# Kernel tuning notes

Hardware: AMD Instinct MI355X
Metric: run time of the kernel (lower is better)

The kernel has to match this reference:

```python
import jax, jax.numpy as jnp
import numpy as np

D_MODEL = 768
N_HEADS = 12
CHUNK = 512
N_LM = 32
BATCH = 2
SEQ = 8192


def setup_inputs() -> dict:
    key = jax.random.key(0)
    ks = jax.random.split(key, 9)
    s = 1.0 / np.sqrt(D_MODEL)
    return {
        "x": jax.random.normal(ks[0], (BATCH, SEQ, D_MODEL), jnp.float32),
        "Wq": jax.random.normal(ks[1], (D_MODEL, D_MODEL), jnp.float32) * s,
        "bq": jax.random.normal(ks[2], (D_MODEL,), jnp.float32) * 0.01,
        "Wk": jax.random.normal(ks[3], (D_MODEL, D_MODEL), jnp.float32) * s,
        "bk": jax.random.normal(ks[4], (D_MODEL,), jnp.float32) * 0.01,
        "Wv": jax.random.normal(ks[5], (D_MODEL, D_MODEL), jnp.float32) * s,
        "bv": jax.random.normal(ks[6], (D_MODEL,), jnp.float32) * 0.01,
        "Wo": jax.random.normal(ks[7], (D_MODEL, D_MODEL), jnp.float32) * s,
        "bo": jax.random.normal(ks[8], (D_MODEL,), jnp.float32) * 0.01,
    }


def reference(x, Wq, bq, Wk, bk, Wv, bv, Wo, bo):
    B, S, D = x.shape
    H, hd = N_HEADS, D // N_HEADS
    scale = hd ** -0.5
    n_chunks = S // CHUNK  # SEQ chosen divisible by CHUNK -> no padding path

    # Global landmarks: mean-pool over N_LM evenly spaced segments
    seg = S // N_LM
    lm = x[:, : seg * N_LM, :].reshape(B, N_LM, seg, D).mean(axis=2)  # (B, L, D)

    # Q over local tokens only
    q = (x @ Wq.T + bq).reshape(B, n_chunks, CHUNK, H, hd)

    # K/V over [landmarks ++ local chunk]
    xc = x.reshape(B, n_chunks, CHUNK, D)
    lm_exp = jnp.broadcast_to(lm[:, None], (B, n_chunks, N_LM, D))
    kv = jnp.concatenate([lm_exp, xc], axis=2)  # (B, n_chunks, N_LM+CHUNK, D)
    k = (kv @ Wk.T + bk).reshape(B, n_chunks, N_LM + CHUNK, H, hd)
    v = (kv @ Wv.T + bv).reshape(B, n_chunks, N_LM + CHUNK, H, hd)

    attn = jnp.einsum("bnqhd,bnkhd->bnhqk", q, k) * scale
    attn = jax.nn.softmax(attn, axis=-1)  # dropout=0 (eval)
    out = jnp.einsum("bnhqk,bnkhd->bnqhd", attn, v).reshape(B, S, D)
    return out @ Wo.T + bo
```

## Files before the change

kernel.cpp:

```cpp
#include <hip/hip_runtime.h>
#include <cstdint>
#include <cstddef>

#define D_MODEL 768
#define N_HEADS 12
#define HEAD_DIM 64
#define CHUNK_SZ 512
#define N_LM 32
#define BATCH 2
#define SEQ 8192
#define N_CH 16
#define SEG 256
#define TOK (BATCH*SEQ)
#define MKV_PAD 16512
#define QSCALE 0.18033688011112042f
#define DEFER_THR 12.0f

typedef unsigned short u16;
typedef __attribute__((ext_vector_type(8))) __bf16 bf16x8;
typedef __attribute__((ext_vector_type(4))) float f32x4;

__device__ __forceinline__ u16 f2bf_rn(float f){
  union { __bf16 b; u16 u; } c; c.b = (__bf16)f; return c.u;
}

__global__ __launch_bounds__(256) void cvt4_kernel(
    const float* __restrict__ w0, const float* __restrict__ w1,
    const float* __restrict__ w2, const float* __restrict__ w3,
    u16* __restrict__ o0, u16* __restrict__ o1, u16* __restrict__ o2, u16* __restrict__ o3)
{
  const int n4 = D_MODEL*D_MODEL/4;
  int i = blockIdx.x*256 + threadIdx.x;
  int sel = i / n4, j = i - sel*n4;
  const float* s = sel==0 ? w0 : sel==1 ? w1 : sel==2 ? w2 : w3;
  u16* o = sel==0 ? o0 : sel==1 ? o1 : sel==2 ? o2 : o3;
  float4 v = reinterpret_cast<const float4*>(s)[j];
  ushort4 p; p.x=f2bf_rn(v.x); p.y=f2bf_rn(v.y); p.z=f2bf_rn(v.z); p.w=f2bf_rn(v.w);
  reinterpret_cast<ushort4*>(o)[j] = p;
}

__global__ void build_xcat_kernel(const float* __restrict__ x, u16* __restrict__ xcat){
  const int total4 = MKV_PAD * D_MODEL / 4;
  const int x4 = TOK * D_MODEL / 4;
  int stride = gridDim.x * blockDim.x;
  for (int i = blockIdx.x*blockDim.x + threadIdx.x; i < total4; i += stride){
    ushort4 o;
    if (i < x4){
      float4 v = reinterpret_cast<const float4*>(x)[i];
      o.x = f2bf_rn(v.x); o.y = f2bf_rn(v.y); o.z = f2bf_rn(v.z); o.w = f2bf_rn(v.w);
    } else { o.x = 0; o.y = 0; o.z = 0; o.w = 0; }
    reinterpret_cast<ushort4*>(xcat)[i] = o;
  }
}

__global__ __launch_bounds__(256) void lm_part_kernel(const float* __restrict__ x, float* __restrict__ lmp){
  int seg = blockIdx.x >> 3, sub = blockIdx.x & 7;
  int b = seg >> 5, l = seg & 31;
  const float* base = x + ((size_t)b*SEQ + (size_t)l*SEG + (size_t)sub*32) * D_MODEL;
  int d = threadIdx.x;
  float a0=0.f, a1=0.f, a2=0.f;
  for (int tt=0; tt<32; ++tt){
    const float* row = base + (size_t)tt*D_MODEL;
    a0 += row[d]; a1 += row[d+256]; a2 += row[d+512];
  }
  float* orow = lmp + (size_t)blockIdx.x * D_MODEL;
  orow[d] = a0; orow[d+256] = a1; orow[d+512] = a2;
}
__global__ __launch_bounds__(256) void lm_final_kernel(const float* __restrict__ lmp, u16* __restrict__ xcat){
  int seg = blockIdx.x;
  int d = threadIdx.x;
  float a0=0.f, a1=0.f, a2=0.f;
  #pragma unroll
  for (int i=0;i<8;i++){
    const float* p = lmp + ((size_t)seg*8 + i)*D_MODEL;
    a0 += p[d]; a1 += p[d+256]; a2 += p[d+512];
  }
  u16* orow = xcat + ((size_t)TOK + seg)*D_MODEL;
  const float inv = 1.f/(float)SEG;
  orow[d] = f2bf_rn(a0*inv); orow[d+256] = f2bf_rn(a1*inv); orow[d+512] = f2bf_rn(a2*inv);
}

template<int OUT_F32, int BIAS_ROW>
__global__ __launch_bounds__(256) void gemm_bt_kernel(
    const u16* __restrict__ A, const u16* __restrict__ Bt,
    const float* __restrict__ bias, void* __restrict__ Cout, int ldc, float scale)
{
  __shared__ u16 As[128][72];
  __shared__ u16 Bs[128][72];
  const int t = threadIdx.x;
  const int lane = t & 63, wid = t >> 6;
  const int wr = wid >> 1, wc = wid & 1;
  const int lr = lane & 15, lg = lane >> 4;
  const size_t row0 = (size_t)blockIdx.y * 128;
  const int col0 = blockIdx.x * 128;

  f32x4 acc[4][4];
  #pragma unroll
  for (int m=0;m<4;m++)
    #pragma unroll
    for (int n=0;n<4;n++) acc[m][n] = f32x4{0.f,0.f,0.f,0.f};

  const int sc = (t & 7) << 3;
  const int sr0 = t >> 3;

  for (int ko = 0; ko < D_MODEL; ko += 64){
    #pragma unroll
    for (int i=0;i<4;i++){
      int r = sr0 + i*32;
      *reinterpret_cast<float4*>(&As[r][sc]) =
        *reinterpret_cast<const float4*>(&A[(row0 + r)*D_MODEL + ko + sc]);
      *reinterpret_cast<float4*>(&Bs[r][sc]) =
        *reinterpret_cast<const float4*>(&Bt[((size_t)col0 + r)*D_MODEL + ko + sc]);
    }
    __syncthreads();
    #pragma unroll
    for (int kk=0;kk<2;kk++){
      bf16x8 af[4], bv[4];
      #pragma unroll
      for (int m=0;m<4;m++)
        af[m] = *reinterpret_cast<const bf16x8*>(&As[wr*64 + m*16 + lr][kk*32 + lg*8]);
      #pragma unroll
      for (int n=0;n<4;n++)
        bv[n] = *reinterpret_cast<const bf16x8*>(&Bs[wc*64 + n*16 + lr][kk*32 + lg*8]);
      #pragma unroll
      for (int m=0;m<4;m++)
        #pragma unroll
        for (int n=0;n<4;n++)
          acc[m][n] = __builtin_amdgcn_mfma_f32_16x16x32_bf16(af[m], bv[n], acc[m][n], 0, 0, 0);
    }
    __syncthreads();
  }

  #pragma unroll
  for (int m=0;m<4;m++){
    #pragma unroll
    for (int n=0;n<4;n++){
      const int col = col0 + wc*64 + n*16 + lr;
      const float bcol = BIAS_ROW ? 0.f : bias[col];
      #pragma unroll
      for (int e=0;e<4;e++){
        size_t row = row0 + wr*64 + m*16 + lg*4 + e;
        float b = BIAS_ROW ? bias[row] : bcol;
        float val = (acc[m][n][e] + b) * scale;
        if (OUT_F32) reinterpret_cast<float*>(Cout)[row*(size_t)ldc + col] = val;
        else         reinterpret_cast<u16*>(Cout)[row*(size_t)ldc + col] = f2bf_rn(val);
      }
    }
  }
}

__global__ __launch_bounds__(256) void gemm_qk_kernel(
    const u16* __restrict__ A, const u16* __restrict__ Wqk,
    const float* __restrict__ bq, const float* __restrict__ bk,
    u16* __restrict__ Qb, u16* __restrict__ Kb)
{
  __shared__ u16 As[128][72];
  __shared__ u16 Bs[128][72];
  const int t = threadIdx.x;
  const int lane = t & 63, wid = t >> 6;
  const int wr = wid >> 1, wc = wid & 1;
  const int lr = lane & 15, lg = lane >> 4;
  const size_t row0 = (size_t)blockIdx.y * 128;
  const int col0 = blockIdx.x * 128;
  const bool isk = col0 >= 768;

  f32x4 acc[4][4];
  #pragma unroll
  for (int m=0;m<4;m++)
    #pragma unroll
    for (int n=0;n<4;n++) acc[m][n] = f32x4{0.f,0.f,0.f,0.f};

  const int sc = (t & 7) << 3;
  const int sr0 = t >> 3;

  for (int ko = 0; ko < D_MODEL; ko += 64){
    #pragma unroll
    for (int i=0;i<4;i++){
      int r = sr0 + i*32;
      *reinterpret_cast<float4*>(&As[r][sc]) =
        *reinterpret_cast<const float4*>(&A[(row0 + r)*D_MODEL + ko + sc]);
      *reinterpret_cast<float4*>(&Bs[r][sc]) =
        *reinterpret_cast<const float4*>(&Wqk[((size_t)col0 + r)*D_MODEL + ko + sc]);
    }
    __syncthreads();
    #pragma unroll
    for (int kk=0;kk<2;kk++){
      bf16x8 af[4], bv[4];
      #pragma unroll
      for (int m=0;m<4;m++)
        af[m] = *reinterpret_cast<const bf16x8*>(&As[wr*64 + m*16 + lr][kk*32 + lg*8]);
      #pragma unroll
      for (int n=0;n<4;n++)
        bv[n] = *reinterpret_cast<const bf16x8*>(&Bs[wc*64 + n*16 + lr][kk*32 + lg*8]);
      #pragma unroll
      for (int m=0;m<4;m++)
        #pragma unroll
        for (int n=0;n<4;n++)
          acc[m][n] = __builtin_amdgcn_mfma_f32_16x16x32_bf16(af[m], bv[n], acc[m][n], 0, 0, 0);
    }
    __syncthreads();
  }

  const float scale = isk ? 1.f : QSCALE;
  u16* dst = isk ? Kb : Qb;
  #pragma unroll
  for (int m=0;m<4;m++){
    #pragma unroll
    for (int n=0;n<4;n++){
      const int col = col0 + wc*64 + n*16 + lr;
      const int ocol = isk ? col - 768 : col;
      const float b = isk ? bk[ocol] : bq[ocol];
      #pragma unroll
      for (int e=0;e<4;e++){
        size_t row = row0 + wr*64 + m*16 + lg*4 + e;
        if (isk || row < TOK){
          float val = (acc[m][n][e] + b) * scale;
          dst[row*D_MODEL + ocol] = f2bf_rn(val);
        }
      }
    }
  }
}

template<int NK>
__device__ __forceinline__ void attn_compute(
    int lr, int lg,
    const u16 (* __restrict__ Ks)[72], const u16 (* __restrict__ Vs)[72],
    u16 (* __restrict__ Pw)[72],
    const bf16x8 (&qf)[2][2], float (&m_run)[2], float (&l_run)[2], f32x4 (&of)[2][4])
{
  constexpr int NCF = NK/16;
  constexpr int NKT = NK/32;

  f32x4 s2[2][NCF];
  #pragma unroll
  for (int c=0;c<NCF;c++){
    bf16x8 kf0 = *reinterpret_cast<const bf16x8*>(&Ks[c*16 + lr][lg*8]);
    bf16x8 kf1 = *reinterpret_cast<const bf16x8*>(&Ks[c*16 + lr][32 + lg*8]);
    #pragma unroll
    for (int r=0;r<2;r++){
      f32x4 s = f32x4{0.f,0.f,0.f,0.f};
      s = __builtin_amdgcn_mfma_f32_16x16x32_bf16(kf0, qf[r][0], s, 0,0,0);
      s = __builtin_amdgcn_mfma_f32_16x16x32_bf16(kf1, qf[r][1], s, 0,0,0);
      s2[r][c] = s;
    }
  }

  bf16x8 vf[NKT][4];
  #pragma unroll
  for (int kt=0;kt<NKT;kt++)
    #pragma unroll
    for (int c=0;c<4;c++)
      vf[kt][c] = *reinterpret_cast<const bf16x8*>(&Vs[c*16 + lr][kt*32 + lg*8]);

  #pragma unroll
  for (int r=0;r<2;r++){
    float tm = s2[r][0][0];
    #pragma unroll
    for (int c=0;c<NCF;c++)
      #pragma unroll
      for (int e=0;e<4;e++) tm = fmaxf(tm, s2[r][c][e]);
    tm = fmaxf(tm, __shfl_xor(tm, 16, 64));
    tm = fmaxf(tm, __shfl_xor(tm, 32, 64));
    if (!__all(tm - m_run[r] <= DEFER_THR)){
      float mnew = fmaxf(m_run[r], tm);
      float al = exp2f(m_run[r] - mnew);
      m_run[r] = mnew;
      l_run[r] *= al;
      #pragma unroll
      for (int c=0;c<4;c++)
        #pragma unroll
        for (int e=0;e<4;e++) of[r][c][e] *= al;
    }
    float ts = 0.f;
    #pragma unroll
    for (int c=0;c<NCF;c++)
      #pragma unroll
      for (int e=0;e<4;e++){
        float p = exp2f(s2[r][c][e] - m_run[r]);
        s2[r][c][e] = p;
        ts += p;
      }
    ts += __shfl_xor(ts, 16, 64);
    ts += __shfl_xor(ts, 32, 64);
    l_run[r] += ts;

    #pragma unroll
    for (int c=0;c<NCF;c++){
      ushort4 pk;
      pk.x = f2bf_rn(s2[r][c][0]); pk.y = f2bf_rn(s2[r][c][1]);
      pk.z = f2bf_rn(s2[r][c][2]); pk.w = f2bf_rn(s2[r][c][3]);
      *reinterpret_cast<ushort4*>(&Pw[lr][c*16 + lg*4]) = pk;
    }
    #pragma unroll
    for (int kt=0;kt<NKT;kt++){
      bf16x8 pf = *reinterpret_cast<const bf16x8*>(&Pw[lr][kt*32 + lg*8]);
      #pragma unroll
      for (int c=0;c<4;c++)
        of[r][c] = __builtin_amdgcn_mfma_f32_16x16x32_bf16(vf[kt][c], pf, of[r][c], 0,0,0);
    }
  }
}

__global__ __launch_bounds__(256) void attn_kernel(
    const u16* __restrict__ Qb, const u16* __restrict__ Kb,
    const u16* __restrict__ Vt, u16* __restrict__ AO)
{
  __shared__ u16 Ks[64][72];
  __shared__ u16 Vs[64][72];
  __shared__ u16 PwAll[4][16][72];

  const int t = threadIdx.x;
  const int lane = t & 63, w = t >> 6;
  const int lr = lane & 15, lg = lane >> 4;
  const int qt = blockIdx.x;
  const int h  = blockIdx.y;
  const int b  = blockIdx.z >> 4, ch = blockIdx.z & 15;
  const size_t tok0 = (size_t)b*SEQ + (size_t)ch*CHUNK_SZ + (size_t)qt*128;
  const size_t bch0 = (size_t)b*SEQ + (size_t)ch*CHUNK_SZ;
  u16 (* __restrict__ Pw)[72] = PwAll[w];

  bf16x8 qf[2][2];
  #pragma unroll
  for (int r=0;r<2;r++)
    #pragma unroll
    for (int kk=0;kk<2;kk++)
      qf[r][kk] = *reinterpret_cast<const bf16x8*>(
          &Qb[(tok0 + w*32 + r*16 + lr)*D_MODEL + (size_t)h*HEAD_DIM + kk*32 + lg*8]);

  float m_run[2] = {-INFINITY, -INFINITY};
  float l_run[2] = {0.f, 0.f};
  f32x4 of[2][4];
  #pragma unroll
  for (int r=0;r<2;r++)
    #pragma unroll
    for (int c=0;c<4;c++) of[r][c] = f32x4{0.f,0.f,0.f,0.f};

  {
    const size_t lmrow0 = (size_t)TOK + (size_t)b*N_LM;
    int key = t >> 3, dc = (t & 7) << 3;
    *reinterpret_cast<bf16x8*>(&Ks[key][dc]) = *reinterpret_cast<const bf16x8*>(
        &Kb[(lmrow0 + key)*D_MODEL + (size_t)h*HEAD_DIM + dc]);
    int d = t >> 2, kc = (t & 3) << 3;
    *reinterpret_cast<bf16x8*>(&Vs[d][kc]) = *reinterpret_cast<const bf16x8*>(
        &Vt[((size_t)h*HEAD_DIM + d)*MKV_PAD + lmrow0 + kc]);
    __syncthreads();
    attn_compute<32>(lr, lg, Ks, Vs, Pw, qf, m_run, l_run, of);
  }

  bf16x8 kreg[2], vreg[2];
  const int key0 = t >> 3, dc0 = (t & 7) << 3;
  const int d0 = t >> 3, kc0 = (t & 7) << 3;
  {
    size_t col0 = bch0;
    kreg[0] = *reinterpret_cast<const bf16x8*>(&Kb[(col0 + key0)*D_MODEL + (size_t)h*HEAD_DIM + dc0]);
    kreg[1] = *reinterpret_cast<const bf16x8*>(&Kb[(col0 + key0 + 32)*D_MODEL + (size_t)h*HEAD_DIM + dc0]);
    vreg[0] = *reinterpret_cast<const bf16x8*>(&Vt[((size_t)h*HEAD_DIM + d0)*MKV_PAD + col0 + kc0]);
    vreg[1] = *reinterpret_cast<const bf16x8*>(&Vt[((size_t)h*HEAD_DIM + d0 + 32)*MKV_PAD + col0 + kc0]);
  }
  for (int tl = 0; tl < 8; ++tl){
    __syncthreads();
    *reinterpret_cast<bf16x8*>(&Ks[key0][dc0])      = kreg[0];
    *reinterpret_cast<bf16x8*>(&Ks[key0 + 32][dc0]) = kreg[1];
    *reinterpret_cast<bf16x8*>(&Vs[d0][kc0])        = vreg[0];
    *reinterpret_cast<bf16x8*>(&Vs[d0 + 32][kc0])   = vreg[1];
    __syncthreads();
    if (tl < 7){
      size_t col0 = bch0 + (size_t)(tl+1)*64;
      kreg[0] = *reinterpret_cast<const bf16x8*>(&Kb[(col0 + key0)*D_MODEL + (size_t)h*HEAD_DIM + dc0]);
      kreg[1] = *reinterpret_cast<const bf16x8*>(&Kb[(col0 + key0 + 32)*D_MODEL + (size_t)h*HEAD_DIM + dc0]);
      vreg[0] = *reinterpret_cast<const bf16x8*>(&Vt[((size_t)h*HEAD_DIM + d0)*MKV_PAD + col0 + kc0]);
      vreg[1] = *reinterpret_cast<const bf16x8*>(&Vt[((size_t)h*HEAD_DIM + d0 + 32)*MKV_PAD + col0 + kc0]);
    }
    attn_compute<64>(lr, lg, Ks, Vs, Pw, qf, m_run, l_run, of);
  }

  #pragma unroll
  for (int r=0;r<2;r++){
    float inv = 1.f / l_run[r];
    size_t row = (tok0 + w*32 + r*16 + lr)*D_MODEL + (size_t)h*HEAD_DIM;
    #pragma unroll
    for (int c=0;c<4;c++){
      ushort4 pk;
      pk.x = f2bf_rn(of[r][c][0]*inv); pk.y = f2bf_rn(of[r][c][1]*inv);
      pk.z = f2bf_rn(of[r][c][2]*inv); pk.w = f2bf_rn(of[r][c][3]*inv);
      *reinterpret_cast<ushort4*>(&AO[row + c*16 + lg*4]) = pk;
    }
  }
}

extern "C" void kernel_launch(void* const* d_in, const int* in_sizes, int n_in,
                              void* d_out, int out_size, void* d_ws, size_t ws_size,
                              hipStream_t stream) {
  const float* x  = (const float*)d_in[0];
  const float* Wq = (const float*)d_in[1];
  const float* bq = (const float*)d_in[2];
  const float* Wk = (const float*)d_in[3];
  const float* bk = (const float*)d_in[4];
  const float* Wv = (const float*)d_in[5];
  const float* bv = (const float*)d_in[6];
  const float* Wo = (const float*)d_in[7];
  const float* bo = (const float*)d_in[8];
  float* out = (float*)d_out;

  const size_t XCAT_OFF = 0;
  const size_t Q_OFF    = 25362432;
  const size_t K_OFF    = 50528256;
  const size_t VT_OFF   = 75890688;
  const size_t AO_OFF   = 101253120;
  const size_t WQ_OFF   = 126418944;
  const size_t WK_OFF   = 127598592;
  const size_t WV_OFF   = 128778240;
  const size_t WO_OFF   = 129957888;
  const size_t TOTAL    = 131137536;
  if (ws_size < TOTAL) return;

  char* ws = (char*)d_ws;
  u16* xcat = (u16*)(ws + XCAT_OFF);
  u16* Qb   = (u16*)(ws + Q_OFF);
  u16* Kb   = (u16*)(ws + K_OFF);
  u16* Vt   = (u16*)(ws + VT_OFF);
  u16* AO   = (u16*)(ws + AO_OFF);
  float* lmp = (float*)(ws + AO_OFF);
  u16* wqkb = (u16*)(ws + WQ_OFF);
  u16* wkb  = (u16*)(ws + WK_OFF);
  u16* wvb  = (u16*)(ws + WV_OFF);
  u16* wob  = (u16*)(ws + WO_OFF);

  dim3 blk(256);
  cvt4_kernel<<<dim3(2304), blk, 0, stream>>>(Wq, Wk, Wv, Wo, wqkb, wkb, wvb, wob);
  build_xcat_kernel<<<dim3(4096), blk, 0, stream>>>(x, xcat);
  lm_part_kernel<<<dim3(512), blk, 0, stream>>>(x, lmp);
  lm_final_kernel<<<dim3(64), blk, 0, stream>>>(lmp, xcat);

  gemm_qk_kernel<<<dim3(12, 129), blk, 0, stream>>>(xcat, wqkb, bq, bk, Qb, Kb);
  gemm_bt_kernel<0,1><<<dim3(129, 6), blk, 0, stream>>>(wvb, xcat, bv, (void*)Vt, MKV_PAD, 1.f);

  attn_kernel<<<dim3(4, 12, 32), blk, 0, stream>>>(Qb, Kb, Vt, AO);

  gemm_bt_kernel<1,0><<<dim3(6, 128), blk, 0, stream>>>(AO, wob, bo, (void*)out, D_MODEL, 1.f);
}
```

Measured before the change: 254.2 us.

## Use direct global-to-LDS loads and XCD-aware block remapping in GEMMs

Replaces register-staged global loads into padded shared memory with global_load_lds direct copies into unpadded LDS tiles, shared across the QK, V and output GEMMs via macros. Grids are flattened to 1D, and block IDs are remapped so consecutive tiles land on the same XCD for better L2 locality. Removing the padding may introduce LDS bank conflicts on fragment reads.

```diff
diff --git a/kernel.cpp b/kernel.cpp
--- a/kernel.cpp
+++ b/kernel.cpp
@@ -24,6 +24,16 @@
   union { __bf16 b; u16 u; } c; c.b = (__bf16)f; return c.u;
 }
 
+#define GLOAD_LDS16(gp, lp) \
+  __builtin_amdgcn_global_load_lds((const __attribute__((address_space(1))) void*)(gp), \
+                                   (__attribute__((address_space(3))) void*)(lp), 16, 0, 0)
+
+__device__ __forceinline__ int xcd_remap(int bid, int nwg){
+  int q = nwg >> 3, r = nwg & 7;
+  int xcd = bid & 7, j = bid >> 3;
+  return (xcd < r ? xcd*(q+1) : r*(q+1) + (xcd-r)*q) + j;
+}
+
 __global__ __launch_bounds__(256) void cvt4_kernel(
     const float* __restrict__ w0, const float* __restrict__ w1,
     const float* __restrict__ w2, const float* __restrict__ w3,
@@ -80,57 +90,54 @@
   orow[d] = f2bf_rn(a0*inv); orow[d+256] = f2bf_rn(a1*inv); orow[d+512] = f2bf_rn(a2*inv);
 }
 
-template<int OUT_F32, int BIAS_ROW>
+#define GEMM_PROLOG                                                                \
+  const int t = threadIdx.x;                                                       \
+  const int lane = t & 63, wid = t >> 6;                                           \
+  const int wr = wid >> 1, wc = wid & 1;                                           \
+  const int lr = lane & 15, lg = lane >> 4;
+
+#define GEMM_MAINLOOP(Aptr, Bptr)                                                  \
+  __shared__ u16 As[128*64];                                                       \
+  __shared__ u16 Bs[128*64];                                                       \
+  const int srow = lane >> 3, scol = (lane & 7) << 3;                              \
+  const u16* ga = (Aptr) + (row0 + srow)*(size_t)D_MODEL + scol;                   \
+  const u16* gb = (Bptr) + ((size_t)col0 + srow)*(size_t)D_MODEL + scol;           \
+  f32x4 acc[4][4];                                                                 \
+  _Pragma("unroll") for (int m=0;m<4;m++)                                          \
+    _Pragma("unroll") for (int n=0;n<4;n++) acc[m][n] = f32x4{0.f,0.f,0.f,0.f};    \
+  for (int ko = 0; ko < D_MODEL; ko += 64){                                        \
+    _Pragma("unroll") for (int i=0;i<4;i++){                                       \
+      int chunk = wid*4 + i;                                                       \
+      GLOAD_LDS16(ga + (size_t)chunk*8*D_MODEL + ko, As + chunk*512);              \
+      GLOAD_LDS16(gb + (size_t)chunk*8*D_MODEL + ko, Bs + chunk*512);              \
+    }                                                                              \
+    __syncthreads();                                                               \
+    _Pragma("unroll") for (int kk=0;kk<2;kk++){                                    \
+      bf16x8 af[4], bv[4];                                                         \
+      _Pragma("unroll") for (int m=0;m<4;m++)                                      \
+        af[m] = *reinterpret_cast<const bf16x8*>(&As[(wr*64 + m*16 + lr)*64 + kk*32 + lg*8]); \
+      _Pragma("unroll") for (int n=0;n<4;n++)                                      \
+        bv[n] = *reinterpret_cast<const bf16x8*>(&Bs[(wc*64 + n*16 + lr)*64 + kk*32 + lg*8]); \
+      _Pragma("unroll") for (int m=0;m<4;m++)                                      \
+        _Pragma("unroll") for (int n=0;n<4;n++)                                    \
+          acc[m][n] = __builtin_amdgcn_mfma_f32_16x16x32_bf16(af[m], bv[n], acc[m][n], 0, 0, 0); \
+    }                                                                              \
+    __syncthreads();                                                               \
+  }
+
+template<int OUT_F32, int BIAS_ROW, int ROWFAST, int NFAST>
 __global__ __launch_bounds__(256) void gemm_bt_kernel(
     const u16* __restrict__ A, const u16* __restrict__ Bt,
     const float* __restrict__ bias, void* __restrict__ Cout, int ldc, float scale)
 {
-  __shared__ u16 As[128][72];
-  __shared__ u16 Bs[128][72];
-  const int t = threadIdx.x;
-  const int lane = t & 63, wid = t >> 6;
-  const int wr = wid >> 1, wc = wid & 1;
-  const int lr = lane & 15, lg = lane >> 4;
-  const size_t row0 = (size_t)blockIdx.y * 128;
-  const int col0 = blockIdx.x * 128;
-
-  f32x4 acc[4][4];
-  #pragma unroll
-  for (int m=0;m<4;m++)
-    #pragma unroll
-    for (int n=0;n<4;n++) acc[m][n] = f32x4{0.f,0.f,0.f,0.f};
-
-  const int sc = (t & 7) << 3;
-  const int sr0 = t >> 3;
-
-  for (int ko = 0; ko < D_MODEL; ko += 64){
-    #pragma unroll
-    for (int i=0;i<4;i++){
-      int r = sr0 + i*32;
-      *reinterpret_cast<float4*>(&As[r][sc]) =
-        *reinterpret_cast<const float4*>(&A[(row0 + r)*D_MODEL + ko + sc]);
-      *reinterpret_cast<float4*>(&Bs[r][sc]) =
-        *reinterpret_cast<const float4*>(&Bt[((size_t)col0 + r)*D_MODEL + ko + sc]);
-    }
-    __syncthreads();
-    #pragma unroll
-    for (int kk=0;kk<2;kk++){
-      bf16x8 af[4], bv[4];
-      #pragma unroll
-      for (int m=0;m<4;m++)
-        af[m] = *reinterpret_cast<const bf16x8*>(&As[wr*64 + m*16 + lr][kk*32 + lg*8]);
-      #pragma unroll
-      for (int n=0;n<4;n++)
-        bv[n] = *reinterpret_cast<const bf16x8*>(&Bs[wc*64 + n*16 + lr][kk*32 + lg*8]);
-      #pragma unroll
-      for (int m=0;m<4;m++)
-        #pragma unroll
-        for (int n=0;n<4;n++)
-          acc[m][n] = __builtin_amdgcn_mfma_f32_16x16x32_bf16(af[m], bv[n], acc[m][n], 0, 0, 0);
-    }
-    __syncthreads();
-  }
-
+  int g = xcd_remap(blockIdx.x, gridDim.x);
+  int rowt, colt;
+  if (ROWFAST){ rowt = g % NFAST; colt = g / NFAST; }
+  else        { colt = g % NFAST; rowt = g / NFAST; }
+  const size_t row0 = (size_t)rowt * 128;
+  const int col0 = colt * 128;
+  GEMM_PROLOG
+  GEMM_MAINLOOP(A, Bt)
   #pragma unroll
   for (int m=0;m<4;m++){
     #pragma unroll
@@ -154,53 +161,13 @@
     const float* __restrict__ bq, const float* __restrict__ bk,
     u16* __restrict__ Qb, u16* __restrict__ Kb)
 {
-  __shared__ u16 As[128][72];
-  __shared__ u16 Bs[128][72];
-  const int t = threadIdx.x;
-  const int lane = t & 63, wid = t >> 6;
-  const int wr = wid >> 1, wc = wid & 1;
-  const int lr = lane & 15, lg = lane >> 4;
-  const size_t row0 = (size_t)blockIdx.y * 128;
-  const int col0 = blockIdx.x * 128;
+  int g = xcd_remap(blockIdx.x, gridDim.x);
+  int colt = g % 12, rowt = g / 12;
+  const size_t row0 = (size_t)rowt * 128;
+  const int col0 = colt * 128;
+  GEMM_PROLOG
+  GEMM_MAINLOOP(A, Wqk)
   const bool isk = col0 >= 768;
-
-  f32x4 acc[4][4];
-  #pragma unroll
-  for (int m=0;m<4;m++)
-    #pragma unroll
-    for (int n=0;n<4;n++) acc[m][n] = f32x4{0.f,0.f,0.f,0.f};
-
-  const int sc = (t & 7) << 3;
-  const int sr0 = t >> 3;
-
-  for (int ko = 0; ko < D_MODEL; ko += 64){
-    #pragma unroll
-    for (int i=0;i<4;i++){
-      int r = sr0 + i*32;
-      *reinterpret_cast<float4*>(&As[r][sc]) =
-        *reinterpret_cast<const float4*>(&A[(row0 + r)*D_MODEL + ko + sc]);
-      *reinterpret_cast<float4*>(&Bs[r][sc]) =
-        *reinterpret_cast<const float4*>(&Wqk[((size_t)col0 + r)*D_MODEL + ko + sc]);
-    }
-    __syncthreads();
-    #pragma unroll
-    for (int kk=0;kk<2;kk++){
-      bf16x8 af[4], bv[4];
-      #pragma unroll
-      for (int m=0;m<4;m++)
-        af[m] = *reinterpret_cast<const bf16x8*>(&As[wr*64 + m*16 + lr][kk*32 + lg*8]);
-      #pragma unroll
-      for (int n=0;n<4;n++)
-        bv[n] = *reinterpret_cast<const bf16x8*>(&Bs[wc*64 + n*16 + lr][kk*32 + lg*8]);
-      #pragma unroll
-      for (int m=0;m<4;m++)
-        #pragma unroll
-        for (int n=0;n<4;n++)
-          acc[m][n] = __builtin_amdgcn_mfma_f32_16x16x32_bf16(af[m], bv[n], acc[m][n], 0, 0, 0);
-    }
-    __syncthreads();
-  }
-
   const float scale = isk ? 1.f : QSCALE;
   u16* dst = isk ? Kb : Qb;
   #pragma unroll
@@ -433,10 +400,10 @@
   lm_part_kernel<<<dim3(512), blk, 0, stream>>>(x, lmp);
   lm_final_kernel<<<dim3(64), blk, 0, stream>>>(lmp, xcat);
 
-  gemm_qk_kernel<<<dim3(12, 129), blk, 0, stream>>>(xcat, wqkb, bq, bk, Qb, Kb);
-  gemm_bt_kernel<0,1><<<dim3(129, 6), blk, 0, stream>>>(wvb, xcat, bv, (void*)Vt, MKV_PAD, 1.f);
+  gemm_qk_kernel<<<dim3(1548), blk, 0, stream>>>(xcat, wqkb, bq, bk, Qb, Kb);
+  gemm_bt_kernel<0,1,1,6><<<dim3(774), blk, 0, stream>>>(wvb, xcat, bv, (void*)Vt, MKV_PAD, 1.f);
 
   attn_kernel<<<dim3(4, 12, 32), blk, 0, stream>>>(Qb, Kb, Vt, AO);
 
-  gemm_bt_kernel<1,0><<<dim3(6, 128), blk, 0, stream>>>(AO, wob, bo, (void*)out, D_MODEL, 1.f);
-}
+  gemm_bt_kernel<1,0,0,6><<<dim3(768), blk, 0, stream>>>(AO, wob, bo, (void*)out, D_MODEL, 1.f);
+}
```

Measured after the change: 268.6 us. 1.06x slower.
